# Optimization experiments

Hardware: AMD Instinct MI355X
Metric: run time of the kernel (lower is better)

Reference implementation:

```python
import jax, jax.numpy as jnp
import numpy as np

OUT, IN, R = 8192, 8192, 16
GROUP = 16
SCALING = 16.0 / 16.0  # lora_alpha / r
# nvfp4 (e2m1) code table: 3 low bits magnitude, bit 3 = sign
NVFP4_LUT = jnp.array([0.0, 0.5, 1.0, 1.5, 2.0, 3.0, 4.0, 6.0,
                       -0.0, -0.5, -1.0, -1.5, -2.0, -3.0, -4.0, -6.0],
                      dtype=jnp.float32)


def setup_inputs() -> dict:
    key = jax.random.key(0)
    k1, k2, k3, k4, k5 = jax.random.split(key, 5)
    x = jax.random.normal(k1, (64, IN), dtype=jnp.float32)
    packed_weight = jax.random.randint(k2, (OUT, IN // 2), 0, 256, dtype=jnp.int32).astype(jnp.uint8)
    # effective block scales (global scale already absorbed, as in _load_prequantized_nvfp4)
    weight_block_scales = (jax.random.uniform(k3, (OUT, IN // GROUP), dtype=jnp.float32) + 0.1) * 0.01
    lora_A = jax.random.normal(k4, (R, IN), dtype=jnp.float32) * (1.0 / np.sqrt(IN))
    lora_B = jax.random.normal(k5, (OUT, R), dtype=jnp.float32) * 0.01
    return {"x": x, "packed_weight": packed_weight,
            "weight_block_scales": weight_block_scales,
            "lora_A": lora_A, "lora_B": lora_B}


def _dequant_nvfp4(packed, block_scales):
    # packed: (OUT, IN//2) uint8, two fp4 codes per byte (low nibble = even index)
    low = (packed & 0xF).astype(jnp.int32)
    high = (packed >> 4).astype(jnp.int32)
    codes = jnp.stack([low, high], axis=-1).reshape(packed.shape[0], -1)  # (OUT, IN)
    vals = NVFP4_LUT[codes]
    O, I = vals.shape
    # per-block scale over groups of GROUP along in_features
    W = (vals.reshape(O, I // GROUP, GROUP) * block_scales[:, :, None]).reshape(O, I)
    return W


def reference(x, packed_weight, weight_block_scales, lora_A, lora_B):
    W = _dequant_nvfp4(packed_weight, weight_block_scales)      # (OUT, IN) fp32
    base = x @ W.T                                              # (B, OUT)
    lora = (x @ lora_A.T) @ lora_B.T                            # (B, OUT)
    return base + SCALING * lora
```

## Files before the change

### kernel.cpp

```cpp
#include <hip/hip_runtime.h>
#include <stdint.h>

#define IN_F   8192
#define OUT_F  8192
#define MB     64
#define RANK   16
#define KSPLIT 16

typedef _Float16 f16x8 __attribute__((ext_vector_type(8)));
typedef _Float16 f16x2 __attribute__((ext_vector_type(2)));
typedef float    f32x4 __attribute__((ext_vector_type(4)));

__device__ __forceinline__ unsigned pk2h(float a, float b) {
    return __builtin_bit_cast(unsigned, __builtin_amdgcn_cvt_pkrtz(a, b));
}

__device__ __forceinline__ f16x8 decode8(unsigned p, unsigned s2) {
    unsigned q  = p >> 4;
    unsigned me = __builtin_amdgcn_perm(0x46444240u, 0x3E3C3800u, p & 0x07070707u);
    unsigned mo = __builtin_amdgcn_perm(0x46444240u, 0x3E3C3800u, q & 0x07070707u);
    unsigned he = ((p & 0x08080808u) << 4) | me;
    unsigned ho = ((q & 0x08080808u) << 4) | mo;
    unsigned bu0 = __builtin_amdgcn_perm(ho, he, 0x040C000Cu);
    unsigned bu1 = __builtin_amdgcn_perm(ho, he, 0x050C010Cu);
    unsigned bu2 = __builtin_amdgcn_perm(ho, he, 0x060C020Cu);
    unsigned bu3 = __builtin_amdgcn_perm(ho, he, 0x070C030Cu);
    f16x2 sv = __builtin_bit_cast(f16x2, s2);
    f16x2 h0 = __builtin_bit_cast(f16x2, bu0) * sv;
    f16x2 h1 = __builtin_bit_cast(f16x2, bu1) * sv;
    f16x2 h2 = __builtin_bit_cast(f16x2, bu2) * sv;
    f16x2 h3 = __builtin_bit_cast(f16x2, bu3) * sv;
    f16x8 b;
    b[0]=h0[0]; b[1]=h0[1]; b[2]=h1[0]; b[3]=h1[1];
    b[4]=h2[0]; b[5]=h2[1]; b[6]=h3[0]; b[7]=h3[1];
    return b;
}

__global__ __launch_bounds__(256) void repack_kernel(
    const void* __restrict__ Wpv, unsigned* __restrict__ W2,
    float* __restrict__ t)
{
    const int tid = threadIdx.x;
    const unsigned U = blockIdx.x * 256 + tid;

    unsigned v = ((const unsigned*)Wpv)[tid & 63];
    const bool fmt1 = (__ballot(v > 255u) == 0ull);

    if (blockIdx.x == 0) {
        for (int i = tid; i < MB * RANK; i += 256) t[i] = 0.f;
    }

    const int lane = U & 63;
    const int s    = (U >> 6) & 15;
    const int w    = (U >> 10) & 3;
    const int by   = (U >> 12) & 63;
    const int ks   = (U >> 18) & 15;
    const int l15  = lane & 15, quad = lane >> 4;
    const int row0 = by * 128 + w * 32 + l15;
    const int e    = ks * 64 + s * 4 + quad;

    unsigned d0, d1;
    if (fmt1) {
        const uint4* in4 = (const uint4*)Wpv;
        uint4 a = in4[(size_t)row0 * 1024 + e];
        uint4 b = in4[(size_t)(row0 + 16) * 1024 + e];
        d0 = (a.x & 0xFFu) | ((a.y & 0xFFu) << 8) | ((a.z & 0xFFu) << 16) | (a.w << 24);
        d1 = (b.x & 0xFFu) | ((b.y & 0xFFu) << 8) | ((b.z & 0xFFu) << 16) | (b.w << 24);
    } else {
        const unsigned* in1 = (const unsigned*)Wpv;
        d0 = in1[(size_t)row0 * 1024 + e];
        d1 = in1[(size_t)(row0 + 16) * 1024 + e];
    }
    uint2 o; o.x = d0; o.y = d1;
    ((uint2*)W2)[U] = o;
}

__global__ __launch_bounds__(256) void prep_kernel(
    const float* __restrict__ x, const float* __restrict__ lora_A,
    uint2* __restrict__ xf2, float* __restrict__ t)
{
    const int m = blockIdx.x, kq = blockIdx.y;
    const int tid = threadIdx.x;
    const int mt = m >> 4, l15 = m & 15;
    float acc[RANK];
#pragma unroll
    for (int r = 0; r < RANK; ++r) acc[r] = 0.f;

    const float4* x4 = (const float4*)(x + (size_t)m * IN_F);
    const float4* A4 = (const float4*)lora_A;
#pragma unroll
    for (int it = 0; it < 2; ++it) {
        int j = kq * 512 + it * 256 + tid;
        float4 xv = x4[j];
        uint2 u;
        u.x = pk2h(xv.x, xv.y);
        u.y = pk2h(xv.z, xv.w);
        int kstep = j >> 3, quad = (j >> 1) & 3, h = j & 1;
        xf2[(size_t)(((kstep * 4 + mt) * 64 + quad * 16 + l15) * 2 + h)] = u;
#pragma unroll
        for (int r = 0; r < RANK; ++r) {
            float4 av = A4[(size_t)r * (IN_F / 4) + j];
            acc[r] += xv.x * av.x + xv.y * av.y + xv.z * av.z + xv.w * av.w;
        }
    }
#pragma unroll
    for (int r = 0; r < RANK; ++r)
#pragma unroll
        for (int off = 32; off > 0; off >>= 1)
            acc[r] += __shfl_down(acc[r], off);

    __shared__ float red[4][RANK];
    int lane = tid & 63, wid = tid >> 6;
    if (lane == 0) {
#pragma unroll
        for (int r = 0; r < RANK; ++r) red[wid][r] = acc[r];
    }
    __syncthreads();
    if (tid < RANK)
        atomicAdd(&t[m * RANK + tid],
                  red[0][tid] + red[1][tid] + red[2][tid] + red[3][tid]);
}

__device__ __forceinline__ float4 lora4(const float* __restrict__ t, int m,
                                        const float* __restrict__ lora_B, int n4) {
    const float4* t4 = (const float4*)(t + m * RANK);
    float4 ta = t4[0], tb = t4[1], tc = t4[2], td = t4[3];
    float4 o;
    float* op = (float*)&o;
#pragma unroll
    for (int j = 0; j < 4; ++j) {
        const float4* B4 = (const float4*)(lora_B + (size_t)(n4 + j) * RANK);
        float4 b0 = B4[0], b1 = B4[1], b2 = B4[2], b3 = B4[3];
        op[j] = ta.x * b0.x + ta.y * b0.y + ta.z * b0.z + ta.w * b0.w
              + tb.x * b1.x + tb.y * b1.y + tb.z * b1.z + tb.w * b1.w
              + tc.x * b2.x + tc.y * b2.y + tc.z * b2.z + tc.w * b2.w
              + td.x * b3.x + td.y * b3.y + td.z * b3.z + td.w * b3.w;
    }
    return o;
}

__global__ __launch_bounds__(256) void lora_kernel(
    const float* __restrict__ t, const float* __restrict__ lora_B,
    float* __restrict__ out)
{
    const int gid = blockIdx.x * 256 + threadIdx.x;
    ((float4*)out)[gid] = lora4(t, gid >> 11, lora_B, (gid & 2047) * 4);
}

__global__ __launch_bounds__(256) void finish_kernel(
    const float* __restrict__ partial, const float* __restrict__ t,
    const float* __restrict__ lora_B, float* __restrict__ out)
{
    const int gid = blockIdx.x * 256 + threadIdx.x;
    float4 p = {0.f, 0.f, 0.f, 0.f};
#pragma unroll
    for (int ksp = 0; ksp < KSPLIT; ++ksp) {
        float4 v = ((const float4*)partial)[(size_t)ksp * (MB * OUT_F / 4) + gid];
        p.x += v.x; p.y += v.y; p.z += v.z; p.w += v.w;
    }
    float4 l = lora4(t, gid >> 11, lora_B, (gid & 2047) * 4);
    p.x += l.x; p.y += l.y; p.z += l.z; p.w += l.w;
    ((float4*)out)[gid] = p;
}

template<int ATOMIC>
__global__ __launch_bounds__(256, 4) void main3_kernel(
    const unsigned* __restrict__ W2,
    const float*    __restrict__ scales,
    const uint4*    __restrict__ xf4,
    float*          __restrict__ dst)
{
    const int tid = threadIdx.x;
    const int lane = tid & 63, w = tid >> 6;
    const int l15 = lane & 15, quad = lane >> 4, qh = quad >> 1;
    const int ks = blockIdx.x, by = blockIdx.y;
    const int n0 = by * 128 + w * 32;
    const int row = n0 + l15;

    unsigned sreg[2][16];
#pragma unroll
    for (int nt = 0; nt < 2; ++nt) {
        const float4* sp = (const float4*)(scales + (size_t)(row + nt * 16) * (IN_F / 16)
                                           + ks * 32);
#pragma unroll
        for (int i = 0; i < 8; ++i) {
            float4 v = sp[i];
            float a = qh ? v.y : v.x, b = qh ? v.w : v.z;
            sreg[nt][2 * i]     = pk2h(a, a);
            sreg[nt][2 * i + 1] = pk2h(b, b);
        }
    }

    f32x4 acc[4][2];
#pragma unroll
    for (int mt = 0; mt < 4; ++mt)
#pragma unroll
        for (int nt = 0; nt < 2; ++nt)
            acc[mt][nt] = (f32x4){0.f, 0.f, 0.f, 0.f};

    const uint2* wp = (const uint2*)W2
                    + (((size_t)(ks * 64 + by) * 4 + w) * 16) * 64 + lane;
    const uint4* xp = xf4 + (size_t)ks * 4096 + lane;

#pragma unroll
    for (int s = 0; s < 16; ++s) {
        uint2 u = wp[s * 64];
        f16x8 afr[4];
#pragma unroll
        for (int mt = 0; mt < 4; ++mt)
            afr[mt] = __builtin_bit_cast(f16x8, xp[(s * 4 + mt) * 64]);
#pragma unroll
        for (int nt = 0; nt < 2; ++nt) {
            unsigned p = nt ? u.y : u.x;
            f16x8 b = decode8(p, sreg[nt][s]);
#pragma unroll
            for (int mt = 0; mt < 4; ++mt)
                acc[mt][nt] = __builtin_amdgcn_mfma_f32_16x16x32_f16(
                    afr[mt], b, acc[mt][nt], 0, 0, 0);
        }
    }

    if (ATOMIC == 0) {
        float* pb = dst + (size_t)ks * (MB * OUT_F);
#pragma unroll
        for (int mt = 0; mt < 4; ++mt)
#pragma unroll
            for (int nt = 0; nt < 2; ++nt)
#pragma unroll
                for (int r = 0; r < 4; ++r)
                    pb[(size_t)(mt * 16 + quad * 4 + r) * OUT_F + n0 + nt * 16 + l15]
                        = acc[mt][nt][r];
    } else {
#pragma unroll
        for (int mt = 0; mt < 4; ++mt)
#pragma unroll
            for (int nt = 0; nt < 2; ++nt)
#pragma unroll
                for (int r = 0; r < 4; ++r)
                    atomicAdd(&dst[(size_t)(mt * 16 + quad * 4 + r) * OUT_F
                                   + n0 + nt * 16 + l15], acc[mt][nt][r]);
    }
}

extern "C" void kernel_launch(void* const* d_in, const int* in_sizes, int n_in,
                              void* d_out, int out_size, void* d_ws, size_t ws_size,
                              hipStream_t stream)
{
    (void)in_sizes; (void)n_in; (void)out_size;
    const float* x      = (const float*)d_in[0];
    const void*  Wp     = (const void*)d_in[1];
    const float* scales = (const float*)d_in[2];
    const float* lora_A = (const float*)d_in[3];
    const float* lora_B = (const float*)d_in[4];
    float* out = (float*)d_out;

    char* ws = (char*)d_ws;
    float* t       = (float*)(ws + 4096);
    uint2* xf      = (uint2*)(ws + 65536);
    float* partial = (float*)(ws + (2u << 20));
    const bool full = ws_size >= ((size_t)67 << 20);
    unsigned* W2 = full ? (unsigned*)(ws + (34u << 20))
                        : (unsigned*)(ws + (2u << 20));

    repack_kernel<<<(OUT_F * (IN_F / 8) / 2) / 256, 256, 0, stream>>>(Wp, W2, t);
    prep_kernel<<<dim3(64, 4), 256, 0, stream>>>(x, lora_A, xf, t);

    if (full) {
        main3_kernel<0><<<dim3(KSPLIT, 64), 256, 0, stream>>>(
            W2, scales, (const uint4*)xf, partial);
        finish_kernel<<<(MB * OUT_F / 4) / 256, 256, 0, stream>>>(
            partial, t, lora_B, out);
    } else {
        lora_kernel<<<(MB * OUT_F / 4) / 256, 256, 0, stream>>>(t, lora_B, out);
        main3_kernel<1><<<dim3(KSPLIT, 64), 256, 0, stream>>>(
            W2, scales, (const uint4*)xf, out);
    }
}
```

Baseline: 260.0 us.

## Fuse weight repack into GEMM via double-buffered LDS staging

Removes the separate repack kernel that rewrote the packed weights into an MFMA-friendly layout. The main kernel now loads raw packed weight chunks from global memory into registers, writes them into a swizzled double-buffered LDS tile, and reads fragments from LDS, prefetching the next chunk while computing. The LoRA t reduction now writes per-kq partials instead of using atomics on a zeroed buffer, which removes the dependency on the repack kernel for zeroing. This saves a full read and write pass over the weights and one launch, at the cost of extra LDS traffic, barriers, and a lower occupancy hint.

New measurement: 239.8 us. 1.08x faster.

```diff
diff --git a/kernel.cpp b/kernel.cpp
--- a/kernel.cpp
+++ b/kernel.cpp
@@ -36,48 +36,15 @@
     return b;
 }
 
-__global__ __launch_bounds__(256) void repack_kernel(
-    const void* __restrict__ Wpv, unsigned* __restrict__ W2,
-    float* __restrict__ t)
-{
-    const int tid = threadIdx.x;
-    const unsigned U = blockIdx.x * 256 + tid;
-
-    unsigned v = ((const unsigned*)Wpv)[tid & 63];
-    const bool fmt1 = (__ballot(v > 255u) == 0ull);
-
-    if (blockIdx.x == 0) {
-        for (int i = tid; i < MB * RANK; i += 256) t[i] = 0.f;
-    }
-
-    const int lane = U & 63;
-    const int s    = (U >> 6) & 15;
-    const int w    = (U >> 10) & 3;
-    const int by   = (U >> 12) & 63;
-    const int ks   = (U >> 18) & 15;
-    const int l15  = lane & 15, quad = lane >> 4;
-    const int row0 = by * 128 + w * 32 + l15;
-    const int e    = ks * 64 + s * 4 + quad;
-
-    unsigned d0, d1;
-    if (fmt1) {
-        const uint4* in4 = (const uint4*)Wpv;
-        uint4 a = in4[(size_t)row0 * 1024 + e];
-        uint4 b = in4[(size_t)(row0 + 16) * 1024 + e];
-        d0 = (a.x & 0xFFu) | ((a.y & 0xFFu) << 8) | ((a.z & 0xFFu) << 16) | (a.w << 24);
-        d1 = (b.x & 0xFFu) | ((b.y & 0xFFu) << 8) | ((b.z & 0xFFu) << 16) | (b.w << 24);
-    } else {
-        const unsigned* in1 = (const unsigned*)Wpv;
-        d0 = in1[(size_t)row0 * 1024 + e];
-        d1 = in1[(size_t)(row0 + 16) * 1024 + e];
-    }
-    uint2 o; o.x = d0; o.y = d1;
-    ((uint2*)W2)[U] = o;
+__device__ __forceinline__ unsigned pack4(uint4 a) {
+    unsigned t0 = __builtin_amdgcn_perm(a.y, a.x, 0x0C0C0400u);
+    unsigned t1 = __builtin_amdgcn_perm(a.w, a.z, 0x0C0C0400u);
+    return __builtin_amdgcn_perm(t1, t0, 0x05040100u);
 }
 
 __global__ __launch_bounds__(256) void prep_kernel(
     const float* __restrict__ x, const float* __restrict__ lora_A,
-    uint2* __restrict__ xf2, float* __restrict__ t)
+    uint2* __restrict__ xf2, float* __restrict__ tp)
 {
     const int m = blockIdx.x, kq = blockIdx.y;
     const int tid = threadIdx.x;
@@ -117,38 +84,50 @@
     }
     __syncthreads();
     if (tid < RANK)
-        atomicAdd(&t[m * RANK + tid],
-                  red[0][tid] + red[1][tid] + red[2][tid] + red[3][tid]);
-}
-
-__device__ __forceinline__ float4 lora4(const float* __restrict__ t, int m,
+        tp[((size_t)kq * MB + m) * RANK + tid] =
+            red[0][tid] + red[1][tid] + red[2][tid] + red[3][tid];
+}
+
+__device__ __forceinline__ float4 lora4(const float* __restrict__ tp, int m,
                                         const float* __restrict__ lora_B, int n4) {
-    const float4* t4 = (const float4*)(t + m * RANK);
-    float4 ta = t4[0], tb = t4[1], tc = t4[2], td = t4[3];
+    float ta[RANK];
+#pragma unroll
+    for (int r = 0; r < RANK; ++r) ta[r] = 0.f;
+#pragma unroll
+    for (int kq = 0; kq < 4; ++kq) {
+        const float4* t4 = (const float4*)(tp + ((size_t)kq * MB + m) * RANK);
+#pragma unroll
+        for (int i = 0; i < 4; ++i) {
+            float4 v = t4[i];
+            ta[4*i+0] += v.x; ta[4*i+1] += v.y; ta[4*i+2] += v.z; ta[4*i+3] += v.w;
+        }
+    }
     float4 o;
     float* op = (float*)&o;
 #pragma unroll
     for (int j = 0; j < 4; ++j) {
         const float4* B4 = (const float4*)(lora_B + (size_t)(n4 + j) * RANK);
-        float4 b0 = B4[0], b1 = B4[1], b2 = B4[2], b3 = B4[3];
-        op[j] = ta.x * b0.x + ta.y * b0.y + ta.z * b0.z + ta.w * b0.w
-              + tb.x * b1.x + tb.y * b1.y + tb.z * b1.z + tb.w * b1.w
-              + tc.x * b2.x + tc.y * b2.y + tc.z * b2.z + tc.w * b2.w
-              + td.x * b3.x + td.y * b3.y + td.z * b3.z + td.w * b3.w;
+        float s = 0.f;
+#pragma unroll
+        for (int i = 0; i < 4; ++i) {
+            float4 b = B4[i];
+            s += ta[4*i+0]*b.x + ta[4*i+1]*b.y + ta[4*i+2]*b.z + ta[4*i+3]*b.w;
+        }
+        op[j] = s;
     }
     return o;
 }
 
 __global__ __launch_bounds__(256) void lora_kernel(
-    const float* __restrict__ t, const float* __restrict__ lora_B,
+    const float* __restrict__ tp, const float* __restrict__ lora_B,
     float* __restrict__ out)
 {
     const int gid = blockIdx.x * 256 + threadIdx.x;
-    ((float4*)out)[gid] = lora4(t, gid >> 11, lora_B, (gid & 2047) * 4);
+    ((float4*)out)[gid] = lora4(tp, gid >> 11, lora_B, (gid & 2047) * 4);
 }
 
 __global__ __launch_bounds__(256) void finish_kernel(
-    const float* __restrict__ partial, const float* __restrict__ t,
+    const float* __restrict__ partial, const float* __restrict__ tp,
     const float* __restrict__ lora_B, float* __restrict__ out)
 {
     const int gid = blockIdx.x * 256 + threadIdx.x;
@@ -158,18 +137,20 @@
         float4 v = ((const float4*)partial)[(size_t)ksp * (MB * OUT_F / 4) + gid];
         p.x += v.x; p.y += v.y; p.z += v.z; p.w += v.w;
     }
-    float4 l = lora4(t, gid >> 11, lora_B, (gid & 2047) * 4);
+    float4 l = lora4(tp, gid >> 11, lora_B, (gid & 2047) * 4);
     p.x += l.x; p.y += l.y; p.z += l.z; p.w += l.w;
     ((float4*)out)[gid] = p;
 }
 
 template<int ATOMIC>
-__global__ __launch_bounds__(256, 4) void main3_kernel(
-    const unsigned* __restrict__ W2,
-    const float*    __restrict__ scales,
-    const uint4*    __restrict__ xf4,
-    float*          __restrict__ dst)
-{
+__global__ __launch_bounds__(256, 3) void main4_kernel(
+    const void*  __restrict__ Wpv,
+    const float* __restrict__ scales,
+    const uint4* __restrict__ xf4,
+    float*       __restrict__ dst)
+{
+    __shared__ __align__(16) unsigned wbuf[2][2048];
+
     const int tid = threadIdx.x;
     const int lane = tid & 63, w = tid >> 6;
     const int l15 = lane & 15, quad = lane >> 4, qh = quad >> 1;
@@ -177,6 +158,9 @@
     const int n0 = by * 128 + w * 32;
     const int row = n0 + l15;
 
+    unsigned dv = ((const unsigned*)Wpv)[lane];
+    const bool fmt1 = (__ballot(dv > 255u) == 0ull);
+
     unsigned sreg[2][16];
 #pragma unroll
     for (int nt = 0; nt < 2; ++nt) {
@@ -184,8 +168,8 @@
                                            + ks * 32);
 #pragma unroll
         for (int i = 0; i < 8; ++i) {
-            float4 v = sp[i];
-            float a = qh ? v.y : v.x, b = qh ? v.w : v.z;
+            float4 vv = sp[i];
+            float a = qh ? vv.y : vv.x, b = qh ? vv.w : vv.z;
             sreg[nt][2 * i]     = pk2h(a, a);
             sreg[nt][2 * i + 1] = pk2h(b, b);
         }
@@ -198,27 +182,82 @@
         for (int nt = 0; nt < 2; ++nt)
             acc[mt][nt] = (f32x4){0.f, 0.f, 0.f, 0.f};
 
-    const uint2* wp = (const uint2*)W2
-                    + (((size_t)(ks * 64 + by) * 4 + w) * 16) * 64 + lane;
-    const uint4* xp = xf4 + (size_t)ks * 4096 + lane;
-
-#pragma unroll
-    for (int s = 0; s < 16; ++s) {
-        uint2 u = wp[s * 64];
-        f16x8 afr[4];
-#pragma unroll
-        for (int mt = 0; mt < 4; ++mt)
-            afr[mt] = __builtin_bit_cast(f16x8, xp[(s * 4 + mt) * 64]);
-#pragma unroll
-        for (int nt = 0; nt < 2; ++nt) {
-            unsigned p = nt ? u.y : u.x;
-            f16x8 b = decode8(p, sreg[nt][s]);
+    const uint4* xp  = xf4 + (size_t)ks * 4096 + lane;
+    const uint4* Wp4 = (const uint4*)Wpv;
+
+    uint4 rg[8];
+
+#define LOADC(c)                                                              \
+    do {                                                                      \
+        if (fmt1) {                                                           \
+            _Pragma("unroll") for (int i = 0; i < 8; ++i) {                   \
+                int rl = (tid >> 4) + i * 16;                                 \
+                rg[i] = Wp4[(size_t)(by * 128 + rl) * 1024                    \
+                            + (ks * 64 + (c) * 16 + (tid & 15))];             \
+            }                                                                 \
+        } else {                                                              \
+            _Pragma("unroll") for (int i = 0; i < 2; ++i) {                   \
+                int rl = (tid >> 2) + i * 64;                                 \
+                rg[i] = Wp4[(size_t)(by * 128 + rl) * 256                     \
+                            + (ks * 16 + (c) * 4 + (tid & 3))];               \
+            }                                                                 \
+        }                                                                     \
+    } while (0)
+
+#define WRITEC(buf)                                                           \
+    do {                                                                      \
+        if (fmt1) {                                                           \
+            int te = tid & 15;                                                \
+            _Pragma("unroll") for (int i = 0; i < 8; ++i) {                   \
+                int rl = (tid >> 4) + i * 16;                                 \
+                wbuf[buf][rl * 16 + (te ^ (rl & 14))] = pack4(rg[i]);         \
+            }                                                                 \
+        } else {                                                              \
+            _Pragma("unroll") for (int i = 0; i < 2; ++i) {                   \
+                int rl = (tid >> 2) + i * 64;                                 \
+                int eb = (tid & 3) * 4;                                       \
+                wbuf[buf][rl * 16 + ((eb + 0) ^ (rl & 14))] = rg[i].x;        \
+                wbuf[buf][rl * 16 + ((eb + 1) ^ (rl & 14))] = rg[i].y;        \
+                wbuf[buf][rl * 16 + ((eb + 2) ^ (rl & 14))] = rg[i].z;        \
+                wbuf[buf][rl * 16 + ((eb + 3) ^ (rl & 14))] = rg[i].w;        \
+            }                                                                 \
+        }                                                                     \
+    } while (0)
+
+    LOADC(0);
+    WRITEC(0);
+    __syncthreads();
+    LOADC(1);
+
+#pragma unroll
+    for (int c = 0; c < 4; ++c) {
+#pragma unroll
+        for (int sc = 0; sc < 4; ++sc) {
+            const int s = c * 4 + sc;
+            f16x8 afr[4];
 #pragma unroll
             for (int mt = 0; mt < 4; ++mt)
-                acc[mt][nt] = __builtin_amdgcn_mfma_f32_16x16x32_f16(
-                    afr[mt], b, acc[mt][nt], 0, 0, 0);
-        }
-    }
+                afr[mt] = __builtin_bit_cast(f16x8, xp[(s * 4 + mt) * 64]);
+#pragma unroll
+            for (int nt = 0; nt < 2; ++nt) {
+                const int rl = w * 32 + nt * 16 + l15;
+                unsigned p = wbuf[c & 1][rl * 16 + ((sc * 4 + quad) ^ (l15 & 14))];
+                f16x8 b = decode8(p, sreg[nt][s]);
+#pragma unroll
+                for (int mt = 0; mt < 4; ++mt)
+                    acc[mt][nt] = __builtin_amdgcn_mfma_f32_16x16x32_f16(
+                        afr[mt], b, acc[mt][nt], 0, 0, 0);
+            }
+        }
+        if (c < 3) {
+            __syncthreads();
+            WRITEC((c + 1) & 1);
+            if (c < 2) LOADC(c + 2);
+            __syncthreads();
+        }
+    }
+#undef LOADC
+#undef WRITEC
 
     if (ATOMIC == 0) {
         float* pb = dst + (size_t)ks * (MB * OUT_F);
@@ -255,24 +294,21 @@
     float* out = (float*)d_out;
 
     char* ws = (char*)d_ws;
-    float* t       = (float*)(ws + 4096);
+    float* tp      = (float*)ws;
     uint2* xf      = (uint2*)(ws + 65536);
     float* partial = (float*)(ws + (2u << 20));
-    const bool full = ws_size >= ((size_t)67 << 20);
-    unsigned* W2 = full ? (unsigned*)(ws + (34u << 20))
-                        : (unsigned*)(ws + (2u << 20));
-
-    repack_kernel<<<(OUT_F * (IN_F / 8) / 2) / 256, 256, 0, stream>>>(Wp, W2, t);
-    prep_kernel<<<dim3(64, 4), 256, 0, stream>>>(x, lora_A, xf, t);
+    const bool full = ws_size >= ((size_t)34 << 20);
+
+    prep_kernel<<<dim3(64, 4), 256, 0, stream>>>(x, lora_A, xf, tp);
 
     if (full) {
-        main3_kernel<0><<<dim3(KSPLIT, 64), 256, 0, stream>>>(
-            W2, scales, (const uint4*)xf, partial);
+        main4_kernel<0><<<dim3(KSPLIT, 64), 256, 0, stream>>>(
+            Wp, scales, (const uint4*)xf, partial);
         finish_kernel<<<(MB * OUT_F / 4) / 256, 256, 0, stream>>>(
-            partial, t, lora_B, out);
+            partial, tp, lora_B, out);
     } else {
-        lora_kernel<<<(MB * OUT_F / 4) / 256, 256, 0, stream>>>(t, lora_B, out);
-        main3_kernel<1><<<dim3(KSPLIT, 64), 256, 0, stream>>>(
-            W2, scales, (const uint4*)xf, out);
-    }
-}
+        lora_kernel<<<(MB * OUT_F / 4) / 256, 256, 0, stream>>>(tp, lora_B, out);
+        main4_kernel<1><<<dim3(KSPLIT, 64), 256, 0, stream>>>(
+            Wp, scales, (const uint4*)xf, out);
+    }
+}
```
